# Performance work log

Hardware: AMD Instinct MI355X
Metric: run time of the kernel (lower is better)

## Reference

```python
import jax, jax.numpy as jnp
import numpy as np

ALPHA = 1.702
LIMIT = 7.0


def setup_inputs() -> dict:
    key = jax.random.key(0)
    ks = jax.random.split(key, 7)
    B, S, H, D, E, TOPK = 2, 2048, 2048, 2048, 8, 4
    T = B * S
    hidden_states = jax.random.normal(ks[0], (B, S, H), dtype=jnp.float32)
    gate_up_proj = jax.random.normal(ks[1], (E, H, 2 * D), dtype=jnp.float32) * 0.02
    gate_up_proj_bias = jax.random.normal(ks[2], (E, 2 * D), dtype=jnp.float32) * 0.02
    down_proj = jax.random.normal(ks[3], (E, D, H), dtype=jnp.float32) * 0.02
    down_proj_bias = jax.random.normal(ks[4], (E, H), dtype=jnp.float32) * 0.02
    rw = jax.random.uniform(ks[5], (T, E), dtype=jnp.float32)
    routing_weights = rw / jnp.sum(rw, axis=-1, keepdims=True)
    router_indices = jax.random.randint(ks[6], (T, TOPK), 0, E, dtype=jnp.int64)
    return {
        "hidden_states": hidden_states,
        "gate_up_proj": gate_up_proj,
        "gate_up_proj_bias": gate_up_proj_bias,
        "down_proj": down_proj,
        "down_proj_bias": down_proj_bias,
        "routing_weights": routing_weights,
        "router_indices": router_indices,
    }


def geglu(gate_up):
    # interleaved layout: gate = [..., 0::2], up = [..., 1::2]
    gate = gate_up[..., 0::2]
    up = gate_up[..., 1::2]
    gate = jnp.minimum(gate, LIMIT)
    up = jnp.clip(up, -LIMIT, LIMIT)
    glu = gate * jax.nn.sigmoid(gate * ALPHA)
    return (up + 1.0) * glu


def reference(hidden_states, gate_up_proj, gate_up_proj_bias, down_proj,
              down_proj_bias, routing_weights, router_indices):
    B, S, H = hidden_states.shape
    x = hidden_states.reshape(-1, H)  # [T, H]
    # per-expert batched GEMM: [E, T, 2D]
    gate_up = jnp.einsum('th,ehd->etd', x, gate_up_proj) + gate_up_proj_bias[:, None, :]
    act = geglu(gate_up)  # [E, T, D]
    out = jnp.einsum('etd,edh->eth', act, down_proj) + down_proj_bias[:, None, :]
    # weight by router probs and sum over experts
    out = out * routing_weights.T[:, :, None]  # [E, T, H]
    out = jnp.sum(out, axis=0)
    return out.reshape(B, S, H)
```

## Files before the change

kernel.cpp:

```cpp
#include <hip/hip_runtime.h>
#include <hip/hip_bf16.h>

#define ALPHA 1.702f
#define GLIMIT 7.0f

typedef __attribute__((ext_vector_type(4))) float f32x4;
typedef __attribute__((ext_vector_type(8))) __bf16 bf16x8;
typedef __attribute__((ext_vector_type(8))) short short8;

typedef __attribute__((address_space(3))) unsigned int as3_uint;
typedef const __attribute__((address_space(1))) unsigned int as1_uint;

__device__ __forceinline__ void async_copy16(void* lds, const void* g) {
    __builtin_amdgcn_global_load_lds((as1_uint*)g, (as3_uint*)lds, 16, 0, 0);
}

__device__ __forceinline__ short f2bf(float f) {
    unsigned u = __float_as_uint(f);
    unsigned r = (u + 0x7fffu + ((u >> 16) & 1u)) >> 16;
    return (short)r;
}

__global__ void cvt_bf16_kernel(const float* __restrict__ src,
                                short* __restrict__ dst, int n4) {
    int i = blockIdx.x * blockDim.x + threadIdx.x;
    if (i < n4) {
        float4 v = reinterpret_cast<const float4*>(src)[i];
        short4 o;
        o.x = f2bf(v.x); o.y = f2bf(v.y); o.z = f2bf(v.z); o.w = f2bf(v.w);
        reinterpret_cast<short4*>(dst)[i] = o;
    }
}

__global__ void transpose_cvt(const float* __restrict__ src,
                              short* __restrict__ dst, int R, int C, int perm) {
    __shared__ float t[64][65];
    const int z  = blockIdx.z;
    const int c0 = blockIdx.x * 64;
    const int r0 = blockIdx.y * 64;
    const float* s = src + (size_t)z * R * C;
    short* d = dst + (size_t)z * R * C;
    const int tid = threadIdx.x;
#pragma unroll
    for (int i = 0; i < 16; ++i) {
        int idx = i * 256 + tid;
        int r = idx >> 6, c = idx & 63;
        t[r][c] = s[(size_t)(r0 + r) * C + c0 + c];
    }
    __syncthreads();
#pragma unroll
    for (int i = 0; i < 16; ++i) {
        int idx = i * 256 + tid;
        int r = idx >> 6, c = idx & 63;
        int rr = c0 + r;
        int rloc = rr & 255;
        int rp = perm ? ((rr & ~255) | ((rloc & 1) << 7) | (rloc >> 1)) : rr;
        d[(size_t)rp * R + r0 + c] = f2bf(t[c][r]);
    }
}


struct Gemm1PSrc {
    const short* A; const short* B;
    __device__ __forceinline__ const short* operator()(int t, int h) const {
        int e = (t >> 5) & 7;
        size_t ko = (size_t)(t & 31) << 6;
        if (h & 2) return B + ((size_t)e << 23) + ((size_t)(h & 1) << 18) + ko;
        return A + ((size_t)(h & 1) << 18) + ko;
    }
};

struct Gemm2Src {
    const short* act; const short* wdt; size_t aoff, boff; int kh;
    __device__ __forceinline__ const short* operator()(int t, int h) const {
        int g = (kh << 7) + t;
        int e = (g >> 5) & 7;
        size_t ko = (size_t)(g & 31) << 6;
        if (h & 2) return wdt + ((size_t)e << 22) + boff + ((size_t)(h & 1) << 18) + ko;
        return act + ((size_t)e << 23) + aoff + ((size_t)(h & 1) << 18) + ko;
    }
};

#define PH_BAR()  __builtin_amdgcn_s_barrier()
#define PH_LGKM() do { asm volatile("s_waitcnt lgkmcnt(0)" ::: "memory"); \
                       __builtin_amdgcn_sched_barrier(0); } while (0)
#define VMW(n)    asm volatile("s_waitcnt vmcnt(" #n ")" ::: "memory")

template <int NT, int SEG, bool DRAIN, typename Src, typename Epi>
__device__ __forceinline__ void gemm_8phase(const Src& src, char* smem,
                                            f32x4 (&acc)[8][4], const Epi& epi) {
    const int tid  = threadIdx.x;
    const int lane = tid & 63;
    const int wid  = tid >> 6;
    const int wr   = wid >> 2;
    const int wcol = wid & 3;
    const int lhi  = lane >> 4;
    const int llo  = lane & 15;

    auto stage = [&](int buf, int h, const short* g) {
        char* dst = smem + buf * 65536 + h * 16384;
        {
            int c = tid, r = c >> 3, s = (c & 7) ^ (r & 7);
            async_copy16(dst + c * 16, g + (size_t)r * 2048 + s * 8);
        }
        {
            int c = tid + 512, r = c >> 3, s = (c & 7) ^ (r & 7);
            async_copy16(dst + c * 16, g + (size_t)r * 2048 + s * 8);
        }
    };
    auto ldfrag = [&](int buf, int h, int row, int slot) {
        return *(const bf16x8*)(smem + buf * 65536 + h * 16384 + row * 128 +
                                ((slot ^ (row & 7)) << 4));
    };

    stage(0, 0, src(0, 0)); stage(0, 2, src(0, 2));
    stage(0, 3, src(0, 3)); stage(0, 1, src(0, 1));
    stage(1, 0, src(1, 0)); stage(1, 2, src(1, 2)); stage(1, 3, src(1, 3));
    VMW(8);
    PH_BAR();

    bf16x8 a[4][2], b[4][2];
#pragma unroll
    for (int n = 0; n < 2; ++n) {
        int row = wcol * 32 + n * 16 + llo;
        b[n][0] = ldfrag(0, 2, row, lhi);
        b[n][1] = ldfrag(0, 2, row, 4 + lhi);
    }

    for (int t = 0; t < NT; ++t) {
        const int cur = t & 1, nxt = cur ^ 1;
#pragma unroll
        for (int m = 0; m < 4; ++m) {
            int row = wr * 64 + m * 16 + llo;
            a[m][0] = ldfrag(cur, 0, row, lhi);
            a[m][1] = ldfrag(cur, 0, row, 4 + lhi);
        }
        if (t + 1 < NT) stage(nxt, 1, src(t + 1, 1));
        PH_BAR(); PH_LGKM();
        __builtin_amdgcn_s_setprio(1);
#pragma unroll
        for (int m = 0; m < 4; ++m)
#pragma unroll
            for (int n = 0; n < 2; ++n)
#pragma unroll
                for (int ks = 0; ks < 2; ++ks)
                    acc[m][n] = __builtin_amdgcn_mfma_f32_16x16x32_bf16(
                        a[m][ks], b[n][ks], acc[m][n], 0, 0, 0);
        __builtin_amdgcn_s_setprio(0);
        PH_BAR();
#pragma unroll
        for (int n = 0; n < 2; ++n) {
            int row = wcol * 32 + n * 16 + llo;
            b[2 + n][0] = ldfrag(cur, 3, row, lhi);
            b[2 + n][1] = ldfrag(cur, 3, row, 4 + lhi);
        }
        if (t + 2 < NT) { stage(cur, 0, src(t + 2, 0)); VMW(10); }
        else if (t + 1 < NT) { VMW(8); }
        else { VMW(0); }
        PH_BAR(); PH_LGKM();
        __builtin_amdgcn_s_setprio(1);
#pragma unroll
        for (int m = 0; m < 4; ++m)
#pragma unroll
            for (int n = 2; n < 4; ++n)
#pragma unroll
                for (int ks = 0; ks < 2; ++ks)
                    acc[m][n] = __builtin_amdgcn_mfma_f32_16x16x32_bf16(
                        a[m][ks], b[n][ks], acc[m][n], 0, 0, 0);
        __builtin_amdgcn_s_setprio(0);
        PH_BAR();
#pragma unroll
        for (int m = 0; m < 4; ++m) {
            int row = wr * 64 + m * 16 + llo;
            a[m][0] = ldfrag(cur, 1, row, lhi);
            a[m][1] = ldfrag(cur, 1, row, 4 + lhi);
        }
        if (t + 2 < NT) stage(cur, 2, src(t + 2, 2));
        PH_BAR(); PH_LGKM();
        __builtin_amdgcn_s_setprio(1);
#pragma unroll
        for (int m = 0; m < 4; ++m)
#pragma unroll
            for (int n = 0; n < 2; ++n)
#pragma unroll
                for (int ks = 0; ks < 2; ++ks)
                    acc[4 + m][n] = __builtin_amdgcn_mfma_f32_16x16x32_bf16(
                        a[m][ks], b[n][ks], acc[4 + m][n], 0, 0, 0);
        __builtin_amdgcn_s_setprio(0);
        PH_BAR();
        if (t + 2 < NT) { stage(cur, 3, src(t + 2, 3)); VMW(8); }
        else if (t + 1 < NT) { VMW(2); }
        else { VMW(0); }
        PH_BAR(); PH_LGKM();
        __builtin_amdgcn_s_setprio(1);
        if (t + 1 < NT) {
#pragma unroll
            for (int n = 0; n < 2; ++n) {
                int row = wcol * 32 + n * 16 + llo;
                b[n][0] = ldfrag(nxt, 2, row, lhi);
                b[n][1] = ldfrag(nxt, 2, row, 4 + lhi);
            }
        }
#pragma unroll
        for (int m = 0; m < 4; ++m)
#pragma unroll
            for (int n = 2; n < 4; ++n)
#pragma unroll
                for (int ks = 0; ks < 2; ++ks)
                    acc[4 + m][n] = __builtin_amdgcn_mfma_f32_16x16x32_bf16(
                        a[m][ks], b[n][ks], acc[4 + m][n], 0, 0, 0);
        __builtin_amdgcn_s_setprio(0);
        PH_BAR();
        if (((t + 1) & (SEG - 1)) == 0) {
            epi(t / SEG, acc);
            if (t + 1 < NT) {
                if (DRAIN) { VMW(0); }
#pragma unroll
                for (int m = 0; m < 8; ++m)
#pragma unroll
                    for (int n = 0; n < 4; ++n)
                        acc[m][n] = (f32x4){0.f, 0.f, 0.f, 0.f};
            }
        }
    }
}

__global__ __launch_bounds__(512, 2) void gemm1_main(
    const short* __restrict__ xb, const short* __restrict__ wgut,
    const float* __restrict__ bias, const float* __restrict__ rwp,
    short* __restrict__ act) {
    __shared__ __align__(16) char smem[131072];
    __shared__ float rws2[2048];
    __shared__ float bias2[2048];
    const int bid = blockIdx.x;
    const int xcd = bid & 7, j = bid >> 3;
    const int n0 = (((xcd << 1) + (j >> 4)) << 8);
    const int m0 = ((j & 15) << 8);
    const int tid  = threadIdx.x;
    const int lane = tid & 63;
    const int wid  = tid >> 6;
    const int wr = wid >> 2, wcol = wid & 3;
    const int lhi = lane >> 4, llo = lane & 15;

    ((float4*)rws2)[tid] = ((const float4*)(rwp + (size_t)m0 * 8))[tid];
    {
        int idx = tid << 2;
        int ei = idx >> 8, c = idx & 255;
        ((float4*)bias2)[tid] =
            *(const float4*)(bias + (size_t)ei * 4096 + n0 + c);
    }

    f32x4 acc[8][4];
#pragma unroll
    for (int m = 0; m < 8; ++m)
#pragma unroll
        for (int n = 0; n < 4; ++n) acc[m][n] = (f32x4){0.f, 0.f, 0.f, 0.f};

    Gemm1PSrc src{ xb + (size_t)m0 * 2048, wgut + (size_t)n0 * 2048 };
    const int a0 = n0 >> 1;

    auto epi = [&](int s, f32x4 (&ac)[8][4]) {
        int e = s & 7;
        short* acte = act + ((size_t)e << 23);
        float bg[2], bu[2];
#pragma unroll
        for (int n = 0; n < 2; ++n) {
            int acol = wcol * 32 + n * 16 + llo;
            bg[n] = bias2[(e << 8) + 2 * acol];
            bu[n] = bias2[(e << 8) + 2 * acol + 1];
        }
        PH_LGKM();
        PH_BAR();
#pragma unroll
        for (int c = 0; c < 4; ++c) {
            char* slot = smem + ((c & 1) ? 32768 : 81920);
#pragma unroll
            for (int mb = 0; mb < 2; ++mb) {
                int m = 2 * c + mb;
                int rowb = (m >> 2) * 128 + wr * 64 + (m & 3) * 16 + (lhi << 2);
#pragma unroll
                for (int n = 0; n < 2; ++n) {
                    int acol = wcol * 32 + n * 16 + llo;
#pragma unroll
                    for (int q = 0; q < 4; ++q) {
                        float g = ac[m][n][q] + bg[n];
                        float u = ac[m][n + 2][q] + bu[n];
                        g = fminf(g, GLIMIT);
                        u = fmaxf(fminf(u, GLIMIT), -GLIMIT);
                        float glu = g / (1.f + __expf(-ALPHA * g));
                        float aa = (u + 1.f) * glu * rws2[(rowb + q) * 8 + e];
                        int lrow = wr * 32 + mb * 16 + (lhi << 2) + q;
                        *(short*)(slot + lrow * 256 +
                                  (((acol << 1) ^ ((lrow & 15) << 4)))) = f2bf(aa);
                    }
                }
            }
            PH_LGKM();
            PH_BAR();
#pragma unroll
            for (int i = 0; i < 2; ++i) {
                int idx = i * 512 + tid;
                int lrow = idx >> 4, g16 = idx & 15;
                int grow = ((c >> 1) << 7) + ((lrow >> 5) << 6) +
                           (((c & 1) * 2 + ((lrow >> 4) & 1)) << 4) + (lrow & 15);
                short8 vv = *(const short8*)(slot + lrow * 256 +
                                             ((g16 ^ (lrow & 15)) << 4));
                __builtin_nontemporal_store(
                    vv, (short8*)(acte + (size_t)(m0 + grow) * 2048 + a0 + g16 * 8));
            }
        }
        PH_BAR();
    };
    gemm_8phase<256, 32, true>(src, smem, acc, epi);
}

__global__ __launch_bounds__(512, 2) void gemm2_8ph(
    const short* __restrict__ act, const short* __restrict__ wdt,
    float* __restrict__ out, float* __restrict__ part) {
    __shared__ __align__(16) char smem[131072];
    const int kh = blockIdx.z;
    int flat = blockIdx.x + (blockIdx.y << 3);
    int swz = (flat & 7) * 16 + (flat >> 3);
    const int n0 = (swz & 7) * 256;
    const int m0 = (swz >> 3) * 256;
    const int tid  = threadIdx.x;
    const int lane = tid & 63;
    const int wid  = tid >> 6;
    const int wr = wid >> 2, wcol = wid & 3;

    f32x4 acc[8][4];
#pragma unroll
    for (int m = 0; m < 8; ++m)
#pragma unroll
        for (int n = 0; n < 4; ++n) acc[m][n] = (f32x4){0.f, 0.f, 0.f, 0.f};

    Gemm2Src src{ act, wdt, (size_t)m0 * 2048, (size_t)n0 * 2048, kh };
    float* dst = (kh == 0) ? out : part;

    auto epi = [&](int, f32x4 (&ac)[8][4]) {
#pragma unroll
        for (int m = 0; m < 8; ++m) {
            int row = m0 + (m >> 2) * 128 + wr * 64 + (m & 3) * 16 + ((lane >> 4) << 2);
#pragma unroll
            for (int n = 0; n < 4; ++n) {
                int col = n0 + (n >> 1) * 128 + wcol * 32 + (n & 1) * 16 + (lane & 15);
#pragma unroll
                for (int q = 0; q < 4; ++q)
                    dst[(size_t)(row + q) * 2048 + col] = ac[m][n][q];
            }
        }
    };
    gemm_8phase<128, 128, false>(src, smem, acc, epi);
}

__global__ __launch_bounds__(256) void reduce_bias(
    const float* __restrict__ p1, const float* __restrict__ rw,
    const float* __restrict__ bd, float* __restrict__ out) {
    const int t = blockIdx.x;
    const int tid = threadIdx.x;
    float rwv[8];
#pragma unroll
    for (int e = 0; e < 8; ++e) rwv[e] = rw[(size_t)t * 8 + e];
    size_t base = (size_t)t * 2048;
#pragma unroll
    for (int i = 0; i < 2; ++i) {
        int h = (tid + i * 256) * 4;
        f32x4 o = *(const f32x4*)(out + base + h);
        f32x4 p = *(const f32x4*)(p1 + base + h);
        o += p;
#pragma unroll
        for (int e = 0; e < 8; ++e) {
            f32x4 bb = *(const f32x4*)(bd + e * 2048 + h);
            o += rwv[e] * bb;
        }
        *(f32x4*)(out + base + h) = o;
    }
}

extern "C" void kernel_launch(void* const* d_in, const int* in_sizes, int n_in,
                              void* d_out, int out_size, void* d_ws, size_t ws_size,
                              hipStream_t stream) {
    const float* x   = (const float*)d_in[0];
    const float* wgu = (const float*)d_in[1];
    const float* bgu = (const float*)d_in[2];
    const float* wd  = (const float*)d_in[3];
    const float* bd  = (const float*)d_in[4];
    const float* rw  = (const float*)d_in[5];
    float* out = (float*)d_out;

    char* ws = (char*)d_ws;
    short* xb   = (short*)(ws);
    short* wgut = (short*)(ws + 16777216);
    float* p1   = (float*)(ws + 16777216);
    short* wdt  = (short*)(ws + 150994944);
    short* actb = (short*)(ws + 218103808);

    cvt_bf16_kernel<<<8192, 256, 0, stream>>>(x, xb, 2097152);
    transpose_cvt<<<dim3(64, 32, 8), 256, 0, stream>>>(wgu, wgut, 2048, 4096, 1);
    transpose_cvt<<<dim3(32, 32, 8), 256, 0, stream>>>(wd, wdt, 2048, 2048, 0);
    gemm1_main<<<256, 512, 0, stream>>>(xb, wgut, bgu, rw, actb);
    gemm2_8ph<<<dim3(8, 16, 2), 512, 0, stream>>>(actb, wdt, out, p1);
    reduce_bias<<<4096, 256, 0, stream>>>(p1, rw, bd, out);
}
```

Before: 929.3 us.

## Replace LDS-staged GEMM1 epilogue with shuffle-based 4x4 transposes and direct stores

The GEMM1 epilogue previously staged the activated tile through shared memory with barriers before writing 16-byte stores. It now does an in-register 4x4 transpose with wave shuffles and writes 8-byte nontemporal stores directly to global memory, removing the LDS round trip and the epilogue barriers. The transpose-convert kernel also writes two bf16 values per store instead of one. The trade-off is narrower global stores and extra shuffle instructions in the epilogue.

Result: slower. 962.5 us (+3.6%).

```diff
diff --git a/kernel.cpp b/kernel.cpp
--- a/kernel.cpp
+++ b/kernel.cpp
@@ -5,6 +5,8 @@
 #define GLIMIT 7.0f
 
 typedef __attribute__((ext_vector_type(4))) float f32x4;
+typedef __attribute__((ext_vector_type(4))) short short4v;
+typedef __attribute__((ext_vector_type(2))) short short2v;
 typedef __attribute__((ext_vector_type(8))) __bf16 bf16x8;
 typedef __attribute__((ext_vector_type(8))) short short8;
 
@@ -49,13 +51,16 @@
     }
     __syncthreads();
 #pragma unroll
-    for (int i = 0; i < 16; ++i) {
+    for (int i = 0; i < 8; ++i) {
         int idx = i * 256 + tid;
-        int r = idx >> 6, c = idx & 63;
+        int r = idx >> 5, c2 = (idx & 31) << 1;
         int rr = c0 + r;
         int rloc = rr & 255;
         int rp = perm ? ((rr & ~255) | ((rloc & 1) << 7) | (rloc >> 1)) : rr;
-        d[(size_t)rp * R + r0 + c] = f2bf(t[c][r]);
+        short2v o;
+        o[0] = f2bf(t[c2][r]);
+        o[1] = f2bf(t[c2 + 1][r]);
+        *(short2v*)(d + (size_t)rp * R + r0 + c2) = o;
     }
 }
 
@@ -241,6 +246,8 @@
     const int wid  = tid >> 6;
     const int wr = wid >> 2, wcol = wid & 3;
     const int lhi = lane >> 4, llo = lane & 15;
+    const int llo4 = lane & 3;
+    const int lbase = lane & ~3;
 
     ((float4*)rws2)[tid] = ((const float4*)(rwp + (size_t)m0 * 8))[tid];
     {
@@ -269,47 +276,36 @@
             bg[n] = bias2[(e << 8) + 2 * acol];
             bu[n] = bias2[(e << 8) + 2 * acol + 1];
         }
-        PH_LGKM();
-        PH_BAR();
-#pragma unroll
-        for (int c = 0; c < 4; ++c) {
-            char* slot = smem + ((c & 1) ? 32768 : 81920);
-#pragma unroll
-            for (int mb = 0; mb < 2; ++mb) {
-                int m = 2 * c + mb;
-                int rowb = (m >> 2) * 128 + wr * 64 + (m & 3) * 16 + (lhi << 2);
-#pragma unroll
-                for (int n = 0; n < 2; ++n) {
-                    int acol = wcol * 32 + n * 16 + llo;
-#pragma unroll
-                    for (int q = 0; q < 4; ++q) {
-                        float g = ac[m][n][q] + bg[n];
-                        float u = ac[m][n + 2][q] + bu[n];
-                        g = fminf(g, GLIMIT);
-                        u = fmaxf(fminf(u, GLIMIT), -GLIMIT);
-                        float glu = g / (1.f + __expf(-ALPHA * g));
-                        float aa = (u + 1.f) * glu * rws2[(rowb + q) * 8 + e];
-                        int lrow = wr * 32 + mb * 16 + (lhi << 2) + q;
-                        *(short*)(slot + lrow * 256 +
-                                  (((acol << 1) ^ ((lrow & 15) << 4)))) = f2bf(aa);
-                    }
+#pragma unroll
+        for (int m = 0; m < 8; ++m) {
+            int rowb_l = (m >> 2) * 128 + wr * 64 + (m & 3) * 16 + (lhi << 2);
+#pragma unroll
+            for (int n = 0; n < 2; ++n) {
+                float v[4];
+#pragma unroll
+                for (int q = 0; q < 4; ++q) {
+                    float g = ac[m][n][q] + bg[n];
+                    float u = ac[m][n + 2][q] + bu[n];
+                    g = fminf(g, GLIMIT);
+                    u = fmaxf(fminf(u, GLIMIT), -GLIMIT);
+                    float glu = g / (1.f + __expf(-ALPHA * g));
+                    v[q] = (u + 1.f) * glu * rws2[(rowb_l + q) * 8 + e];
                 }
+                float o[4];
+#pragma unroll
+                for (int k = 0; k < 4; ++k) {
+                    float sv = v[(llo4 + 4 - k) & 3];
+                    o[(llo4 + k) & 3] = __shfl(sv, lbase + ((llo4 + k) & 3));
+                }
+                int row = m0 + rowb_l + llo4;
+                int col = a0 + wcol * 32 + n * 16 + (llo & 12);
+                short4v ov;
+#pragma unroll
+                for (int q = 0; q < 4; ++q) ov[q] = f2bf(o[q]);
+                __builtin_nontemporal_store(
+                    ov, (short4v*)(acte + (size_t)row * 2048 + col));
             }
-            PH_LGKM();
-            PH_BAR();
-#pragma unroll
-            for (int i = 0; i < 2; ++i) {
-                int idx = i * 512 + tid;
-                int lrow = idx >> 4, g16 = idx & 15;
-                int grow = ((c >> 1) << 7) + ((lrow >> 5) << 6) +
-                           (((c & 1) * 2 + ((lrow >> 4) & 1)) << 4) + (lrow & 15);
-                short8 vv = *(const short8*)(slot + lrow * 256 +
-                                             ((g16 ^ (lrow & 15)) << 4));
-                __builtin_nontemporal_store(
-                    vv, (short8*)(acte + (size_t)(m0 + grow) * 2048 + a0 + g16 * 8));
-            }
-        }
-        PH_BAR();
+        }
     };
     gemm_8phase<256, 32, true>(src, smem, acc, epi);
 }
```
